# Performance work log

Measured on AMD Instinct MI355X. Metric: run time of the kernel, lower is better.

Reference implementation:

```python
import jax, jax.numpy as jnp
import numpy as np

EMBED_DIM = 1024
NUM_HEADS = 16
HEAD_DIM = EMBED_DIM // NUM_HEADS
ROPE_BASE = 10000.0


def _rope_cos_sin(seq_len, head_dim, dtype):
    # Standard RoPE (ESM-style rotate_half): freqs outer(t, inv_freq), emb = cat(freqs, freqs)
    inv_freq = 1.0 / (ROPE_BASE ** (jnp.arange(0, head_dim, 2, dtype=jnp.float32) / head_dim))
    t = jnp.arange(seq_len, dtype=jnp.float32)
    freqs = jnp.einsum('s,d->sd', t, inv_freq)          # [s, d/2]
    emb = jnp.concatenate([freqs, freqs], axis=-1)      # [s, d]
    return jnp.cos(emb).astype(dtype), jnp.sin(emb).astype(dtype)


def _rotate_half(x):
    x1, x2 = jnp.split(x, 2, axis=-1)
    return jnp.concatenate([-x2, x1], axis=-1)


def _apply_rope(x, cos, sin):
    # x: [b, h, s, d]; cos/sin: [s, d] broadcast over b, h
    return x * cos + _rotate_half(x) * sin


def setup_inputs() -> dict:
    key = jax.random.key(0)
    ks = jax.random.split(key, 5)
    b, s, e = 4, 2048, EMBED_DIM
    scale = 1.0 / np.sqrt(e)
    x = jax.random.normal(ks[0], (b, s, e), dtype=jnp.float32)
    Wqkv = jax.random.normal(ks[1], (e, 3 * e), dtype=jnp.float32) * scale
    bqkv = jnp.zeros((3 * e,), dtype=jnp.float32)
    Wo = jax.random.normal(ks[2], (e, e), dtype=jnp.float32) * scale
    bo = jnp.zeros((e,), dtype=jnp.float32)
    return {"x": x, "Wqkv": Wqkv, "bqkv": bqkv, "Wo": Wo, "bo": bo}


def reference(x, Wqkv, bqkv, Wo, bo):
    b, s, e = x.shape
    h, d = NUM_HEADS, HEAD_DIM
    qkv = jnp.einsum('bse,ef->bsf', x, Wqkv) + bqkv          # [b, s, 3e]
    q, k, v = jnp.split(qkv, 3, axis=-1)
    # b s (h d) -> b h s d
    q = q.reshape(b, s, h, d).transpose(0, 2, 1, 3)
    k = k.reshape(b, s, h, d).transpose(0, 2, 1, 3)
    v = v.reshape(b, s, h, d).transpose(0, 2, 1, 3)
    cos, sin = _rope_cos_sin(s, d, x.dtype)
    q = _apply_rope(q, cos, sin)
    k = _apply_rope(k, cos, sin)
    # scaled dot product attention (no mask, no dropout, non-causal)
    scores = jnp.einsum('bhqd,bhkd->bhqk', q, k) / jnp.asarray(np.sqrt(d), x.dtype)
    attn = jax.nn.softmax(scores, axis=-1)
    out = jnp.einsum('bhqk,bhkd->bhqd', attn, v)             # [b, h, s, d]
    out = out.transpose(0, 2, 1, 3).reshape(b, s, e)         # b h s d -> b s (h d)
    return jnp.einsum('bse,ef->bsf', out, Wo) + bo
```

## Files before the change

kernel.cpp:

```cpp
#include <hip/hip_runtime.h>
#include <stdint.h>
#include <stddef.h>

typedef __bf16 bf16;
typedef __attribute__((ext_vector_type(8))) __bf16 bf16x8;
typedef __attribute__((ext_vector_type(4))) __bf16 bf16x4;
typedef __attribute__((ext_vector_type(4))) float f32x4;
typedef __attribute__((ext_vector_type(16))) float f32x16;
typedef __attribute__((ext_vector_type(4))) float float4v;
typedef __attribute__((ext_vector_type(4))) uint32_t u32x4;

#define BATCH 4
#define SEQ   2048
#define EMB   1024
#define NH    16
#define HD    64
#define F3    3072

#define MFMA16(a, b, c) __builtin_amdgcn_mfma_f32_16x16x32_bf16((a), (b), (c), 0, 0, 0)
#define MFMA32(a, b, c) __builtin_amdgcn_mfma_f32_32x32x16_bf16((a), (b), (c), 0, 0, 0)

__device__ __forceinline__ float exp2_fast(float x) {
  return __builtin_amdgcn_exp2f(x);
}

__device__ __forceinline__ void gload_lds16(const bf16* g, bf16* l) {
  __builtin_amdgcn_global_load_lds(
      (const __attribute__((address_space(1))) uint32_t*)g,
      (__attribute__((address_space(3))) uint32_t*)l, 16, 0, 0);
}

__device__ __forceinline__ void transpose_tile32(const float* __restrict__ in,
                                                 bf16* __restrict__ out,
                                                 int R, int C, int bx, int by) {
  __shared__ bf16 tile[32][33];
  const int tx = threadIdx.x & 31;
  const int ty = threadIdx.x >> 5;
  const int c0 = bx * 32, r0 = by * 32;
#pragma unroll
  for (int kk = 0; kk < 4; ++kk) {
    int r = ty + kk * 8;
    tile[r][tx] = (bf16)in[(size_t)(r0 + r) * C + c0 + tx];
  }
  __syncthreads();
#pragma unroll
  for (int kk = 0; kk < 4; ++kk) {
    int r = ty + kk * 8;
    out[(size_t)(c0 + r) * R + r0 + tx] = tile[tx][r];
  }
}

__global__ __launch_bounds__(256) void prep_kernel(const float* __restrict__ x_raw,
                                                   bf16* __restrict__ xb,
                                                   const float* __restrict__ wqkv_raw,
                                                   bf16* __restrict__ wqkvT,
                                                   float* __restrict__ cosT,
                                                   float* __restrict__ sinT) {
  const int blk = blockIdx.x;
  if (blk < 8192) {
    int i = blk * 256 + threadIdx.x;
    float4v v = ((const float4v*)x_raw)[i];
    bf16x4 o;
#pragma unroll
    for (int k = 0; k < 4; ++k) o[k] = (bf16)v[k];
    ((bf16x4*)xb)[i] = o;
  } else if (blk < 11264) {
    int idx = blk - 8192;
    transpose_tile32(wqkv_raw, wqkvT, EMB, F3, idx % 96, idx / 96);
  } else {
    int idx = (blk - 11264) * 256 + threadIdx.x;
    int pos = idx >> 5, d1 = idx & 31;
    float inv = powf(10000.0f, -(float)(2 * d1) / 64.0f);
    float th = (float)pos * inv;
    cosT[idx] = cosf(th);
    sinT[idx] = sinf(th);
  }
}

__global__ __launch_bounds__(256) void transpose_f32_bf16(const float* __restrict__ in,
                                                          bf16* __restrict__ out,
                                                          int R, int C) {
  transpose_tile32(in, out, R, C, blockIdx.x, blockIdx.y);
}

__device__ __forceinline__ void gemm128_core(bf16* lds,
                                             const bf16* __restrict__ Abase,
                                             const bf16* __restrict__ Bbase,
                                             f32x4 (&acc)[4][4]) {
  const int tid = threadIdx.x;
  const int w = tid >> 6, lane = tid & 63;
  const int lhi = lane >> 4, llo = lane & 15, l7 = llo & 15 & 7;
  const int wr = w >> 2, wc = w & 3;
  const int srow = lane >> 3;
  const int sk16 = (lane & 7) ^ srow;
  const size_t g_lane = (size_t)(w * 16 + srow) * EMB + sk16 * 8;
  bf16* ldsw = lds + w * 1024;

  const int ka0 = (lhi * 8) ^ (l7 << 3);
  const int ka1 = (32 + lhi * 8) ^ (l7 << 3);
  const int arow = (wr * 64 + llo) * 64;
  const int brow = ((wc & 1) * 64 + llo) * 64;
  const int bsel = wc >> 1;

#pragma unroll
  for (int i = 0; i < 4; ++i)
#pragma unroll
    for (int j = 0; j < 4; ++j) acc[i][j] = (f32x4){0.f, 0.f, 0.f, 0.f};

#define STAGE(baseptr, slot)                              \
  do {                                                    \
    const bf16* _b = (baseptr);                           \
    bf16* _l = ldsw + (slot) * 8192;                      \
    gload_lds16(_b + g_lane, _l);                         \
    gload_lds16(_b + g_lane + 8 * EMB, _l + 512);         \
  } while (0)

  STAGE(Abase, 0);
  STAGE(Bbase, 1);
  STAGE(Bbase + 128 * EMB, 2);
  STAGE(Abase + 64, 3);
  STAGE(Bbase + 64, 4);
  STAGE(Bbase + 128 * EMB + 64, 5);
  asm volatile("s_waitcnt vmcnt(6)" ::: "memory");
  __builtin_amdgcn_s_barrier();

  int s = 0;
#pragma unroll 1
  for (int t = 0; t < 16; ++t) {
    const bf16* ldsA = lds + s * 8192 + arow;
    const bf16* ldsB = lds + (s + 1 + bsel) * 8192 + brow;
    const int k2 = (t + 2) * 64;
    int st2 = s + 6;
    if (st2 >= 9) st2 -= 9;
    bf16x8 a[4][2], b0[2][2], b1[2][2];

#pragma unroll
    for (int i = 0; i < 4; ++i) {
      a[i][0] = *(const bf16x8*)(ldsA + i * 1024 + ka0);
      a[i][1] = *(const bf16x8*)(ldsA + i * 1024 + ka1);
    }
#pragma unroll
    for (int j = 0; j < 2; ++j) {
      b0[j][0] = *(const bf16x8*)(ldsB + j * 1024 + ka0);
      b0[j][1] = *(const bf16x8*)(ldsB + j * 1024 + ka1);
    }
    if (t < 14) {
      STAGE(Abase + k2, st2);
      STAGE(Bbase + k2, st2 + 1);
    }
    __builtin_amdgcn_s_barrier();
    asm volatile("s_waitcnt lgkmcnt(0)" ::: "memory");
    __builtin_amdgcn_sched_barrier(0);
    __builtin_amdgcn_s_setprio(1);
#pragma unroll
    for (int i = 0; i < 4; ++i)
#pragma unroll
      for (int j = 0; j < 2; ++j) {
        acc[i][j] = MFMA16(a[i][0], b0[j][0], acc[i][j]);
        acc[i][j] = MFMA16(a[i][1], b0[j][1], acc[i][j]);
      }
    __builtin_amdgcn_s_setprio(0);
    __builtin_amdgcn_s_barrier();

#pragma unroll
    for (int j = 0; j < 2; ++j) {
      b1[j][0] = *(const bf16x8*)(ldsB + 2048 + j * 1024 + ka0);
      b1[j][1] = *(const bf16x8*)(ldsB + 2048 + j * 1024 + ka1);
    }
    if (t < 14) STAGE(Bbase + 128 * EMB + k2, st2 + 2);
    __builtin_amdgcn_s_barrier();
    asm volatile("s_waitcnt lgkmcnt(0)" ::: "memory");
    __builtin_amdgcn_sched_barrier(0);
    __builtin_amdgcn_s_setprio(1);
#pragma unroll
    for (int i = 0; i < 4; ++i)
#pragma unroll
      for (int j = 0; j < 2; ++j) {
        acc[i][2 + j] = MFMA16(a[i][0], b1[j][0], acc[i][2 + j]);
        acc[i][2 + j] = MFMA16(a[i][1], b1[j][1], acc[i][2 + j]);
      }
    __builtin_amdgcn_s_setprio(0);
    if (t < 14) {
      asm volatile("s_waitcnt vmcnt(6)" ::: "memory");
    } else if (t == 14) {
      asm volatile("s_waitcnt vmcnt(0)" ::: "memory");
    }
    if (t < 15) __builtin_amdgcn_s_barrier();

    s += 3;
    if (s >= 9) s -= 9;
  }
#undef STAGE
}

__global__ __launch_bounds__(512, 2) void qkv128_kernel(
    const bf16* __restrict__ x, const bf16* __restrict__ wT,
    const float* __restrict__ bias, bf16* __restrict__ qo, bf16* __restrict__ ko,
    bf16* __restrict__ vo, const float* __restrict__ cosT,
    const float* __restrict__ sinT) {
  extern __shared__ __align__(16) bf16 ldsb[];
  const int orig = blockIdx.x;
  const int wg = (orig & 7) * 96 + (orig >> 3);
  const int bx = wg % 12, by = wg / 12;
  const int row_a0 = by * 128, row_b0 = bx * 256;

  f32x4 acc[4][4];
  gemm128_core(ldsb, x + (size_t)row_a0 * EMB, wT + (size_t)row_b0 * EMB, acc);

  const int tid = threadIdx.x;
  const int w = tid >> 6, lane = tid & 63;
  const int lhi = lane >> 4, llo = lane & 15;
  const int wr = w >> 2, wc = w & 3;

  const int f0 = row_b0 + wc * 64;
  const int part = f0 >> 10;
  const int hh = (f0 & 1023) >> 6;
  const int m_base = row_a0 + wr * 64;

  float bvals[4];
#pragma unroll
  for (int j = 0; j < 4; ++j) bvals[j] = bias[f0 + j * 16 + llo];

  if (part == 2) {
#pragma unroll
    for (int mi = 0; mi < 4; ++mi) {
      int m0 = m_base + mi * 16 + lhi * 4;
      int bb = m0 >> 11, pos0 = m0 & 2047;
#pragma unroll
      for (int j = 0; j < 4; ++j) {
        int dd = j * 16 + llo;
        bf16x4 pk;
#pragma unroll
        for (int r = 0; r < 4; ++r) pk[r] = (bf16)(acc[mi][j][r] + bvals[j]);
        *(bf16x4*)(vo + ((size_t)(bb * NH + hh) * HD + dd) * SEQ + pos0) = pk;
      }
    }
  } else {
    bf16* dst = (part == 0) ? qo : ko;
    const float qs = (part == 0) ? 0.18033688f : 1.0f;
#pragma unroll
    for (int mi = 0; mi < 4; ++mi) {
#pragma unroll
      for (int r = 0; r < 4; ++r) {
        int m = m_base + mi * 16 + lhi * 4 + r;
        int bb = m >> 11, pos = m & 2047;
        size_t base = ((size_t)(bb * NH + hh) * SEQ + pos) * HD;
#pragma unroll
        for (int j = 0; j < 2; ++j) {
          int d1 = j * 16 + llo;
          float x1 = acc[mi][j][r] + bvals[j];
          float x2 = acc[mi][j + 2][r] + bvals[j + 2];
          float cth = cosT[pos * 32 + d1];
          float sth = sinT[pos * 32 + d1];
          dst[base + d1] = (bf16)((x1 * cth - x2 * sth) * qs);
          dst[base + d1 + 32] = (bf16)((x2 * cth + x1 * sth) * qs);
        }
      }
    }
  }
}

__global__ __launch_bounds__(512, 2) void outproj128_kernel(
    const bf16* __restrict__ a_in, const bf16* __restrict__ wT,
    const float* __restrict__ bo, float* __restrict__ out) {
  extern __shared__ __align__(16) bf16 ldsb[];
  const int orig = blockIdx.x;
  const int wg = (orig & 7) * 32 + (orig >> 3);
  const int bx = wg % 4, by = wg / 4;
  const int row_a0 = by * 128, row_b0 = bx * 256;

  f32x4 acc[4][4];
  gemm128_core(ldsb, a_in + (size_t)row_a0 * EMB, wT + (size_t)row_b0 * EMB, acc);

  const int tid = threadIdx.x;
  const int w = tid >> 6, lane = tid & 63;
  const int lhi = lane >> 4, llo = lane & 15;
  const int wr = w >> 2, wc = w & 3;

  const int col0 = row_b0 + wc * 64;
  const int m_base = row_a0 + wr * 64;
  float bvals[4];
#pragma unroll
  for (int j = 0; j < 4; ++j) bvals[j] = bo[col0 + j * 16 + llo];
#pragma unroll
  for (int mi = 0; mi < 4; ++mi) {
#pragma unroll
    for (int r = 0; r < 4; ++r) {
      int m = m_base + mi * 16 + lhi * 4 + r;
#pragma unroll
      for (int j = 0; j < 4; ++j)
        out[(size_t)m * EMB + col0 + j * 16 + llo] = acc[mi][j][r] + bvals[j];
    }
  }
}

__global__ __launch_bounds__(512, 2) void attn32_kernel(const bf16* __restrict__ q,
                                                        const bf16* __restrict__ k,
                                                        const bf16* __restrict__ vT,
                                                        bf16* __restrict__ o) {
  __shared__ __align__(16) bf16 smem[16384];

  const int tid = threadIdx.x, w = tid >> 6, lane = tid & 63;
  const int l31 = lane & 31, hi = lane >> 5;
  const int bidx = blockIdx.x;
  const int vblk = (bidx & 7) * 64 + (bidx >> 3);
  const int qt = vblk & 7, bh = vblk >> 3;
  const bf16* qbase = q + (size_t)bh * SEQ * HD + qt * 256 * HD;
  const bf16* kbase = k + (size_t)bh * SEQ * HD;
  const bf16* vbase = vT + (size_t)bh * HD * SEQ;

  const int rowc = lane >> 3;
  const int sw8 = (lane & 7) ^ rowc;

  bf16x8 qf[4];
  {
    const bf16* qrow = qbase + (size_t)(w * 32 + l31) * HD;
#pragma unroll
    for (int c = 0; c < 4; ++c) qf[c] = *(const bf16x8*)(qrow + c * 16 + hi * 8);
  }

  if (w < 4) {
#pragma unroll
    for (int c = 0; c < 2; ++c) {
      int ch = w * 2 + c, row = ch * 8 + rowc;
      gload_lds16(kbase + (size_t)row * HD + sw8 * 8, &smem[ch * 512]);
    }
  } else {
#pragma unroll
    for (int c = 0; c < 2; ++c) {
      int ch = (w - 4) * 2 + c, row = ch * 8 + rowc;
      gload_lds16(vbase + (size_t)row * SEQ + sw8 * 8, &smem[8192 + ch * 512]);
    }
  }
  __syncthreads();

  float rsum = 0.f;
  f32x16 oacc[2];
#pragma unroll
  for (int r = 0; r < 16; ++r) { oacc[0][r] = 0.f; oacc[1][r] = 0.f; }

  const int swz = (l31 & 7);

  for (int kb = 0; kb < 32; ++kb) {
    bf16* Kc = smem + (kb & 1) * 4096;
    bf16* Vc = smem + 8192 + (kb & 1) * 4096;
    if (kb < 31) {
      int kpos = (kb + 1) * 64;
      if (w < 4) {
        bf16* Kn = smem + ((kb + 1) & 1) * 4096;
#pragma unroll
        for (int c = 0; c < 2; ++c) {
          int ch = w * 2 + c, row = ch * 8 + rowc;
          gload_lds16(kbase + (size_t)(kpos + row) * HD + sw8 * 8, &Kn[ch * 512]);
        }
      } else {
        bf16* Vn = smem + 8192 + ((kb + 1) & 1) * 4096;
#pragma unroll
        for (int c = 0; c < 2; ++c) {
          int ch = (w - 4) * 2 + c, row = ch * 8 + rowc;
          gload_lds16(vbase + (size_t)row * SEQ + kpos + sw8 * 8, &Vn[ch * 512]);
        }
      }
    }

    f32x16 st0, st1;
#pragma unroll
    for (int r = 0; r < 16; ++r) { st0[r] = 0.f; st1[r] = 0.f; }
    __builtin_amdgcn_s_setprio(1);
#pragma unroll
    for (int c = 0; c < 4; ++c) {
      bf16x8 kf0 = *(const bf16x8*)&Kc[l31 * 64 + (((c * 2 + hi) ^ swz) * 8)];
      bf16x8 kf1 = *(const bf16x8*)&Kc[(32 + l31) * 64 + (((c * 2 + hi) ^ swz) * 8)];
      st0 = MFMA32(kf0, qf[c], st0);
      st1 = MFMA32(kf1, qf[c], st1);
    }
    __builtin_amdgcn_s_setprio(0);

#pragma unroll
    for (int r = 0; r < 16; ++r) {
      st0[r] = exp2_fast(st0[r]);
      st1[r] = exp2_fast(st1[r]);
    }
    {
      float a0 = 0.f, a1 = 0.f, a2 = 0.f, a3 = 0.f;
#pragma unroll
      for (int r = 0; r < 16; r += 4) {
        a0 += st0[r];     a1 += st0[r + 1];
        a2 += st0[r + 2]; a3 += st0[r + 3];
      }
#pragma unroll
      for (int r = 0; r < 16; r += 4) {
        a0 += st1[r];     a1 += st1[r + 1];
        a2 += st1[r + 2]; a3 += st1[r + 3];
      }
      rsum += (a0 + a1) + (a2 + a3);
    }

    bf16x8 pa[4];
#pragma unroll
    for (int tt = 0; tt < 2; ++tt) {
#pragma unroll
      for (int c1 = 0; c1 < 2; ++c1) {
        float s0 = tt ? st1[c1 * 8 + 0] : st0[c1 * 8 + 0];
        float s1 = tt ? st1[c1 * 8 + 1] : st0[c1 * 8 + 1];
        float s2 = tt ? st1[c1 * 8 + 2] : st0[c1 * 8 + 2];
        float s3 = tt ? st1[c1 * 8 + 3] : st0[c1 * 8 + 3];
        float s4 = tt ? st1[c1 * 8 + 4] : st0[c1 * 8 + 4];
        float s5 = tt ? st1[c1 * 8 + 5] : st0[c1 * 8 + 5];
        float s6 = tt ? st1[c1 * 8 + 6] : st0[c1 * 8 + 6];
        float s7 = tt ? st1[c1 * 8 + 7] : st0[c1 * 8 + 7];
        uint32_t a0, a1, b0, b1;
        asm("v_cvt_pk_bf16_f32 %0, %1, %2" : "=v"(a0) : "v"(s0), "v"(s1));
        asm("v_cvt_pk_bf16_f32 %0, %1, %2" : "=v"(a1) : "v"(s2), "v"(s3));
        asm("v_cvt_pk_bf16_f32 %0, %1, %2" : "=v"(b0) : "v"(s4), "v"(s5));
        asm("v_cvt_pk_bf16_f32 %0, %1, %2" : "=v"(b1) : "v"(s6), "v"(s7));
        asm("v_permlane32_swap_b32 %0, %1" : "+v"(a0), "+v"(b0));
        asm("v_permlane32_swap_b32 %0, %1" : "+v"(a1), "+v"(b1));
        u32x4 uv = {a0, a1, b0, b1};
        pa[tt * 2 + c1] = __builtin_bit_cast(bf16x8, uv);
      }
    }

    __builtin_amdgcn_s_setprio(1);
#pragma unroll
    for (int c = 0; c < 4; ++c) {
      bf16x8 v0 = *(const bf16x8*)&Vc[l31 * 64 + (((c * 2 + hi) ^ swz) * 8)];
      bf16x8 v1 = *(const bf16x8*)&Vc[(32 + l31) * 64 + (((c * 2 + hi) ^ swz) * 8)];
      oacc[0] = MFMA32(pa[c], v0, oacc[0]);
      oacc[1] = MFMA32(pa[c], v1, oacc[1]);
    }
    __builtin_amdgcn_s_setprio(0);

    __syncthreads();
  }

  rsum += __shfl_xor(rsum, 32);
  const int bb = bh >> 4, hh = bh & 15;
#pragma unroll
  for (int r = 0; r < 16; ++r) {
    int qrow = (r & 3) + 8 * (r >> 2) + 4 * hi;
    float inv = 1.0f / __shfl(rsum, qrow);
    int pos = qt * 256 + w * 32 + qrow;
    size_t base = ((size_t)bb * SEQ + pos) * EMB + hh * HD;
    o[base + l31] = (bf16)(oacc[0][r] * inv);
    o[base + 32 + l31] = (bf16)(oacc[1][r] * inv);
  }
}

extern "C" void kernel_launch(void* const* d_in, const int* in_sizes, int n_in,
                              void* d_out, int out_size, void* d_ws, size_t ws_size,
                              hipStream_t stream) {
  const float* x_raw = (const float*)d_in[0];
  const float* wqkv_raw = (const float*)d_in[1];
  const float* bqkv = (const float*)d_in[2];
  const float* wo_raw = (const float*)d_in[3];
  const float* bo = (const float*)d_in[4];
  float* out = (float*)d_out;

  char* ws = (char*)d_ws;
  bf16* qw = (bf16*)(ws);
  bf16* kw = (bf16*)(ws + 16777216);
  bf16* vw = (bf16*)(ws + 33554432);
  bf16* wqkvT = (bf16*)(ws + 50331648);
  float* cosT = (float*)(ws + 56623104);
  float* sinT = (float*)(ws + 56885248);
  bf16* ow = (bf16*)(ws + 50331648);
  bf16* woT = (bf16*)(ws);
  bf16* xb = (bf16*)d_out;

  static bool attr_set = false;
  if (!attr_set) {
    (void)hipFuncSetAttribute((const void*)qkv128_kernel,
                              hipFuncAttributeMaxDynamicSharedMemorySize, 163840);
    (void)hipFuncSetAttribute((const void*)outproj128_kernel,
                              hipFuncAttributeMaxDynamicSharedMemorySize, 163840);
    attr_set = true;
  }

  prep_kernel<<<11520, 256, 0, stream>>>(x_raw, xb, wqkv_raw, wqkvT, cosT, sinT);

  qkv128_kernel<<<dim3((BATCH * SEQ / 128) * (F3 / 256)), 512, 147456, stream>>>(
      xb, wqkvT, bqkv, qw, kw, vw, cosT, sinT);
  attn32_kernel<<<dim3(BATCH * NH * (SEQ / 256)), 512, 0, stream>>>(qw, kw, vw, ow);

  transpose_f32_bf16<<<dim3(EMB / 32, EMB / 32), 256, 0, stream>>>(wo_raw, woT, EMB, EMB);
  outproj128_kernel<<<dim3((BATCH * SEQ / 128) * (EMB / 256)), 512, 147456, stream>>>(
      ow, woT, bo, out);
}
```

Measured before the change: 259.3 us.

## Shrink GEMM tiles to 64x256 with simple double-buffered LDS pipeline

Replaces the 128x256 GEMM core, which used a 9-slot triple-stage LDS ring and split B halves, with a 64x256 tile using two LDS buffers and one barrier per k-step. Grid sizes double for both the QKV and output projections and dynamic LDS drops from 147456 to 81920 bytes. This raises block count and may let more blocks share a CU. In exchange each block reuses A and B less, global traffic per FLOP rises, and prefetch depth drops from two stages to one with a full vmcnt(0) wait every iteration.

```diff
diff --git a/kernel.cpp b/kernel.cpp
--- a/kernel.cpp
+++ b/kernel.cpp
@@ -83,129 +83,100 @@
   transpose_tile32(in, out, R, C, blockIdx.x, blockIdx.y);
 }
 
-__device__ __forceinline__ void gemm128_core(bf16* lds,
-                                             const bf16* __restrict__ Abase,
-                                             const bf16* __restrict__ Bbase,
-                                             f32x4 (&acc)[4][4]) {
+__device__ __forceinline__ void gemm64_core(bf16* lds,
+                                            const bf16* __restrict__ Abase,
+                                            const bf16* __restrict__ Bbase,
+                                            f32x4 (&acc)[2][4]) {
   const int tid = threadIdx.x;
   const int w = tid >> 6, lane = tid & 63;
-  const int lhi = lane >> 4, llo = lane & 15, l7 = llo & 15 & 7;
+  const int lhi = lane >> 4, llo = lane & 15, l7 = llo & 7;
   const int wr = w >> 2, wc = w & 3;
   const int srow = lane >> 3;
   const int sk16 = (lane & 7) ^ srow;
-  const size_t g_lane = (size_t)(w * 16 + srow) * EMB + sk16 * 8;
-  bf16* ldsw = lds + w * 1024;
+  const size_t gA_lane = (size_t)(w * 8 + srow) * EMB + sk16 * 8;
+  const size_t gB_lane = (size_t)(w * 16 + srow) * EMB + sk16 * 8;
 
   const int ka0 = (lhi * 8) ^ (l7 << 3);
   const int ka1 = (32 + lhi * 8) ^ (l7 << 3);
-  const int arow = (wr * 64 + llo) * 64;
-  const int brow = ((wc & 1) * 64 + llo) * 64;
-  const int bsel = wc >> 1;
-
-#pragma unroll
-  for (int i = 0; i < 4; ++i)
+  const int arow = (wr * 32 + llo) * 64;
+  const int brow = (wc * 64 + llo) * 64;
+
+#pragma unroll
+  for (int i = 0; i < 2; ++i)
 #pragma unroll
     for (int j = 0; j < 4; ++j) acc[i][j] = (f32x4){0.f, 0.f, 0.f, 0.f};
 
-#define STAGE(baseptr, slot)                              \
-  do {                                                    \
-    const bf16* _b = (baseptr);                           \
-    bf16* _l = ldsw + (slot) * 8192;                      \
-    gload_lds16(_b + g_lane, _l);                         \
-    gload_lds16(_b + g_lane + 8 * EMB, _l + 512);         \
+#define ASTAGE(baseptr, c) \
+  gload_lds16((baseptr) + gA_lane, lds + (c) * 20480 + w * 512)
+#define BSTAGE(baseptr, ldsoff)                               \
+  do {                                                        \
+    bf16* _l = lds + (ldsoff) + w * 1024;                     \
+    gload_lds16((baseptr) + gB_lane, _l);                     \
+    gload_lds16((baseptr) + gB_lane + 8 * EMB, _l + 512);     \
   } while (0)
 
-  STAGE(Abase, 0);
-  STAGE(Bbase, 1);
-  STAGE(Bbase + 128 * EMB, 2);
-  STAGE(Abase + 64, 3);
-  STAGE(Bbase + 64, 4);
-  STAGE(Bbase + 128 * EMB + 64, 5);
-  asm volatile("s_waitcnt vmcnt(6)" ::: "memory");
+  ASTAGE(Abase, 0);
+  BSTAGE(Bbase, 4096);
+  BSTAGE(Bbase + 128 * EMB, 4096 + 8192);
+  asm volatile("s_waitcnt vmcnt(0)" ::: "memory");
   __builtin_amdgcn_s_barrier();
 
-  int s = 0;
 #pragma unroll 1
   for (int t = 0; t < 16; ++t) {
-    const bf16* ldsA = lds + s * 8192 + arow;
-    const bf16* ldsB = lds + (s + 1 + bsel) * 8192 + brow;
-    const int k2 = (t + 2) * 64;
-    int st2 = s + 6;
-    if (st2 >= 9) st2 -= 9;
-    bf16x8 a[4][2], b0[2][2], b1[2][2];
-
-#pragma unroll
-    for (int i = 0; i < 4; ++i) {
+    const int cur = t & 1;
+    const bf16* ldsA = lds + cur * 20480 + arow;
+    const bf16* ldsB = lds + cur * 20480 + 4096 + brow;
+    if (t < 15) {
+      const int alt = cur ^ 1;
+      const int k1 = (t + 1) * 64;
+      ASTAGE(Abase + k1, alt);
+      BSTAGE(Bbase + k1, alt * 20480 + 4096);
+      BSTAGE(Bbase + k1 + 128 * EMB, alt * 20480 + 4096 + 8192);
+    }
+    bf16x8 a[2][2], b[4][2];
+#pragma unroll
+    for (int i = 0; i < 2; ++i) {
       a[i][0] = *(const bf16x8*)(ldsA + i * 1024 + ka0);
       a[i][1] = *(const bf16x8*)(ldsA + i * 1024 + ka1);
     }
 #pragma unroll
-    for (int j = 0; j < 2; ++j) {
-      b0[j][0] = *(const bf16x8*)(ldsB + j * 1024 + ka0);
-      b0[j][1] = *(const bf16x8*)(ldsB + j * 1024 + ka1);
-    }
-    if (t < 14) {
-      STAGE(Abase + k2, st2);
-      STAGE(Bbase + k2, st2 + 1);
-    }
-    __builtin_amdgcn_s_barrier();
+    for (int j = 0; j < 4; ++j) {
+      b[j][0] = *(const bf16x8*)(ldsB + j * 1024 + ka0);
+      b[j][1] = *(const bf16x8*)(ldsB + j * 1024 + ka1);
+    }
     asm volatile("s_waitcnt lgkmcnt(0)" ::: "memory");
     __builtin_amdgcn_sched_barrier(0);
     __builtin_amdgcn_s_setprio(1);
 #pragma unroll
-    for (int i = 0; i < 4; ++i)
-#pragma unroll
-      for (int j = 0; j < 2; ++j) {
-        acc[i][j] = MFMA16(a[i][0], b0[j][0], acc[i][j]);
-        acc[i][j] = MFMA16(a[i][1], b0[j][1], acc[i][j]);
+    for (int i = 0; i < 2; ++i)
+#pragma unroll
+      for (int j = 0; j < 4; ++j) {
+        acc[i][j] = MFMA16(a[i][0], b[j][0], acc[i][j]);
+        acc[i][j] = MFMA16(a[i][1], b[j][1], acc[i][j]);
       }
     __builtin_amdgcn_s_setprio(0);
-    __builtin_amdgcn_s_barrier();
-
-#pragma unroll
-    for (int j = 0; j < 2; ++j) {
-      b1[j][0] = *(const bf16x8*)(ldsB + 2048 + j * 1024 + ka0);
-      b1[j][1] = *(const bf16x8*)(ldsB + 2048 + j * 1024 + ka1);
-    }
-    if (t < 14) STAGE(Bbase + 128 * EMB + k2, st2 + 2);
-    __builtin_amdgcn_s_barrier();
-    asm volatile("s_waitcnt lgkmcnt(0)" ::: "memory");
-    __builtin_amdgcn_sched_barrier(0);
-    __builtin_amdgcn_s_setprio(1);
-#pragma unroll
-    for (int i = 0; i < 4; ++i)
-#pragma unroll
-      for (int j = 0; j < 2; ++j) {
-        acc[i][2 + j] = MFMA16(a[i][0], b1[j][0], acc[i][2 + j]);
-        acc[i][2 + j] = MFMA16(a[i][1], b1[j][1], acc[i][2 + j]);
-      }
-    __builtin_amdgcn_s_setprio(0);
-    if (t < 14) {
-      asm volatile("s_waitcnt vmcnt(6)" ::: "memory");
-    } else if (t == 14) {
+    if (t < 15) {
       asm volatile("s_waitcnt vmcnt(0)" ::: "memory");
-    }
-    if (t < 15) __builtin_amdgcn_s_barrier();
-
-    s += 3;
-    if (s >= 9) s -= 9;
-  }
-#undef STAGE
-}
-
-__global__ __launch_bounds__(512, 2) void qkv128_kernel(
+      __builtin_amdgcn_s_barrier();
+    }
+  }
+#undef ASTAGE
+#undef BSTAGE
+}
+
+__global__ __launch_bounds__(512, 2) void qkv64_kernel(
     const bf16* __restrict__ x, const bf16* __restrict__ wT,
     const float* __restrict__ bias, bf16* __restrict__ qo, bf16* __restrict__ ko,
     bf16* __restrict__ vo, const float* __restrict__ cosT,
     const float* __restrict__ sinT) {
   extern __shared__ __align__(16) bf16 ldsb[];
   const int orig = blockIdx.x;
-  const int wg = (orig & 7) * 96 + (orig >> 3);
+  const int wg = (orig & 7) * 192 + (orig >> 3);
   const int bx = wg % 12, by = wg / 12;
-  const int row_a0 = by * 128, row_b0 = bx * 256;
-
-  f32x4 acc[4][4];
-  gemm128_core(ldsb, x + (size_t)row_a0 * EMB, wT + (size_t)row_b0 * EMB, acc);
+  const int row_a0 = by * 64, row_b0 = bx * 256;
+
+  f32x4 acc[2][4];
+  gemm64_core(ldsb, x + (size_t)row_a0 * EMB, wT + (size_t)row_b0 * EMB, acc);
 
   const int tid = threadIdx.x;
   const int w = tid >> 6, lane = tid & 63;
@@ -215,7 +186,7 @@
   const int f0 = row_b0 + wc * 64;
   const int part = f0 >> 10;
   const int hh = (f0 & 1023) >> 6;
-  const int m_base = row_a0 + wr * 64;
+  const int m_base = row_a0 + wr * 32;
 
   float bvals[4];
 #pragma unroll
@@ -223,7 +194,7 @@
 
   if (part == 2) {
 #pragma unroll
-    for (int mi = 0; mi < 4; ++mi) {
+    for (int mi = 0; mi < 2; ++mi) {
       int m0 = m_base + mi * 16 + lhi * 4;
       int bb = m0 >> 11, pos0 = m0 & 2047;
 #pragma unroll
@@ -239,7 +210,7 @@
     bf16* dst = (part == 0) ? qo : ko;
     const float qs = (part == 0) ? 0.18033688f : 1.0f;
 #pragma unroll
-    for (int mi = 0; mi < 4; ++mi) {
+    for (int mi = 0; mi < 2; ++mi) {
 #pragma unroll
       for (int r = 0; r < 4; ++r) {
         int m = m_base + mi * 16 + lhi * 4 + r;
@@ -260,17 +231,17 @@
   }
 }
 
-__global__ __launch_bounds__(512, 2) void outproj128_kernel(
+__global__ __launch_bounds__(512, 2) void outproj64_kernel(
     const bf16* __restrict__ a_in, const bf16* __restrict__ wT,
     const float* __restrict__ bo, float* __restrict__ out) {
   extern __shared__ __align__(16) bf16 ldsb[];
   const int orig = blockIdx.x;
-  const int wg = (orig & 7) * 32 + (orig >> 3);
+  const int wg = (orig & 7) * 64 + (orig >> 3);
   const int bx = wg % 4, by = wg / 4;
-  const int row_a0 = by * 128, row_b0 = bx * 256;
-
-  f32x4 acc[4][4];
-  gemm128_core(ldsb, a_in + (size_t)row_a0 * EMB, wT + (size_t)row_b0 * EMB, acc);
+  const int row_a0 = by * 64, row_b0 = bx * 256;
+
+  f32x4 acc[2][4];
+  gemm64_core(ldsb, a_in + (size_t)row_a0 * EMB, wT + (size_t)row_b0 * EMB, acc);
 
   const int tid = threadIdx.x;
   const int w = tid >> 6, lane = tid & 63;
@@ -278,12 +249,12 @@
   const int wr = w >> 2, wc = w & 3;
 
   const int col0 = row_b0 + wc * 64;
-  const int m_base = row_a0 + wr * 64;
+  const int m_base = row_a0 + wr * 32;
   float bvals[4];
 #pragma unroll
   for (int j = 0; j < 4; ++j) bvals[j] = bo[col0 + j * 16 + llo];
 #pragma unroll
-  for (int mi = 0; mi < 4; ++mi) {
+  for (int mi = 0; mi < 2; ++mi) {
 #pragma unroll
     for (int r = 0; r < 4; ++r) {
       int m = m_base + mi * 16 + lhi * 4 + r;
@@ -470,20 +441,20 @@
 
   static bool attr_set = false;
   if (!attr_set) {
-    (void)hipFuncSetAttribute((const void*)qkv128_kernel,
+    (void)hipFuncSetAttribute((const void*)qkv64_kernel,
                               hipFuncAttributeMaxDynamicSharedMemorySize, 163840);
-    (void)hipFuncSetAttribute((const void*)outproj128_kernel,
+    (void)hipFuncSetAttribute((const void*)outproj64_kernel,
                               hipFuncAttributeMaxDynamicSharedMemorySize, 163840);
     attr_set = true;
   }
 
   prep_kernel<<<11520, 256, 0, stream>>>(x_raw, xb, wqkv_raw, wqkvT, cosT, sinT);
 
-  qkv128_kernel<<<dim3((BATCH * SEQ / 128) * (F3 / 256)), 512, 147456, stream>>>(
+  qkv64_kernel<<<dim3((BATCH * SEQ / 64) * (F3 / 256)), 512, 81920, stream>>>(
       xb, wqkvT, bqkv, qw, kw, vw, cosT, sinT);
   attn32_kernel<<<dim3(BATCH * NH * (SEQ / 256)), 512, 0, stream>>>(qw, kw, vw, ow);
 
   transpose_f32_bf16<<<dim3(EMB / 32, EMB / 32), 256, 0, stream>>>(wo_raw, woT, EMB, EMB);
-  outproj128_kernel<<<dim3((BATCH * SEQ / 128) * (EMB / 256)), 512, 147456, stream>>>(
+  outproj64_kernel<<<dim3((BATCH * SEQ / 64) * (EMB / 256)), 512, 81920, stream>>>(
       ow, woT, bo, out);
 }
```

Measured after the change: 249.5 us. 1.04x faster.
